# Performance work log

Measured on AMD Instinct MI355X. Metric: run time of the kernel, lower is better.

The kernel has to match this reference:

```python
import jax, jax.numpy as jnp
import numpy as np


def setup_inputs() -> dict:
    key = jax.random.key(0)
    ks = jax.random.split(key, 4)
    B, T, I, H = 64, 1024, 256, 512
    s = 1.0 / np.sqrt(I + H)  # torch Linear default init scale
    xs = jax.random.normal(ks[0], (B, T, I), dtype=jnp.float32)
    Wz = jax.random.uniform(ks[1], (I + H, H), jnp.float32, -s, s)
    Wr = jax.random.uniform(ks[2], (I + H, H), jnp.float32, -s, s)
    Wh = jax.random.uniform(ks[3], (I + H, H), jnp.float32, -s, s)
    bz = jnp.zeros((H,), jnp.float32)
    br = jnp.zeros((H,), jnp.float32)
    bh = jnp.zeros((H,), jnp.float32)
    return {"xs": xs, "Wz": Wz, "bz": bz, "Wr": Wr, "br": br, "Wh": Wh, "bh": bh}


def reference(xs, Wz, bz, Wr, br, Wh, bh):
    B, T, I = xs.shape
    H = Wz.shape[1]
    # split weights into input / hidden blocks so per-step work avoids concat
    Wz_x, Wz_h = Wz[:I], Wz[I:]
    Wr_x, Wr_h = Wr[:I], Wr[I:]
    Wh_x, Wh_h = Wh[:I], Wh[I:]
    # precompute all input projections in one big GEMM per gate: [B,T,H]
    xz = jnp.einsum('bti,ih->bth', xs, Wz_x) + bz
    xr = jnp.einsum('bti,ih->bth', xs, Wr_x) + br
    xh = jnp.einsum('bti,ih->bth', xs, Wh_x) + bh

    def step(h, inp):
        xz_t, xr_t, xh_t = inp
        zt = jax.nn.sigmoid(xz_t + h @ Wz_h)
        rt = jax.nn.sigmoid(xr_t + h @ Wr_h)
        ht = jnp.tanh(xh_t + (rt * h) @ Wh_h)
        h_next = (1 - zt) * h + zt * ht
        return h_next, h_next

    h0 = jnp.zeros((B, H), xs.dtype)
    # scan over time: inputs as [T, B, H]
    xs_t = (jnp.swapaxes(xz, 0, 1), jnp.swapaxes(xr, 0, 1), jnp.swapaxes(xh, 0, 1))
    h_last, hs = jax.lax.scan(step, h0, xs_t)
    return jnp.swapaxes(hs, 0, 1), h_last
```

## Files before the change

kernel.cpp:

```cpp
#include <hip/hip_runtime.h>
#include <cmath>

typedef __bf16 bf16x8 __attribute__((ext_vector_type(8)));
typedef float  f32x4  __attribute__((ext_vector_type(4)));
typedef unsigned long long u64;
typedef u64 u64x2 __attribute__((ext_vector_type(2)));

#define T_STEPS 1024
#define I_DIM   256
#define H_DIM   512
#define B_TOT   64
#define NBT     4
#define NCT     32
#define BT      16
#define CT      16
#define FDOM    64

__device__ __forceinline__ f32x4 mfma16(bf16x8 a, bf16x8 b, f32x4 c) {
    return __builtin_amdgcn_mfma_f32_16x16x32_bf16(a, b, c, 0, 0, 0);
}

__device__ __forceinline__ bf16x8 cvt8r(float4 a, float4 b) {
    bf16x8 f;
    f[0] = (__bf16)a.x; f[1] = (__bf16)a.y; f[2] = (__bf16)a.z; f[3] = (__bf16)a.w;
    f[4] = (__bf16)b.x; f[5] = (__bf16)b.y; f[6] = (__bf16)b.z; f[7] = (__bf16)b.w;
    return f;
}

__device__ __forceinline__ int ld_flag(const int* p) {
    return __hip_atomic_load(p, __ATOMIC_RELAXED, __HIP_MEMORY_SCOPE_AGENT);
}
__device__ __forceinline__ void st_flag(int* p, int v) {
    __hip_atomic_store(p, v, __ATOMIC_RELAXED, __HIP_MEMORY_SCOPE_AGENT);
}
__device__ __forceinline__ void st_u32(unsigned* p, unsigned v) {
    __hip_atomic_store(p, v, __ATOMIC_RELAXED, __HIP_MEMORY_SCOPE_AGENT);
}
__device__ __forceinline__ bf16x8 ld_frag16(const __bf16* p) {
    u64x2 v;
    v.x = __hip_atomic_load((const u64*)p,     __ATOMIC_RELAXED, __HIP_MEMORY_SCOPE_AGENT);
    v.y = __hip_atomic_load((const u64*)p + 1, __ATOMIC_RELAXED, __HIP_MEMORY_SCOPE_AGENT);
    return __builtin_bit_cast(bf16x8, v);
}

__device__ __forceinline__ void wait32(const int* fdom, int target) {
    const int* p = fdom + (threadIdx.x & 31);
    for (int g = 0; g < (1 << 22); ++g) {
        int v = ld_flag(p);
        if (__ballot(v >= target) == ~0ull) break;
    }
    asm volatile("" ::: "memory");
}

__device__ __forceinline__ void drain_vm() {
    __builtin_amdgcn_s_waitcnt(0x0f70);
}

__global__ __launch_bounds__(256, 1) void gru_persist(
    const float* __restrict__ xs,
    const float* __restrict__ Wz, const float* __restrict__ bz,
    const float* __restrict__ Wr, const float* __restrict__ br,
    const float* __restrict__ Wh, const float* __restrict__ bh,
    float* __restrict__ out,
    __bf16* hbuf, __bf16* rhbuf, int* flag_h, int* flag_r)
{
    const int bid  = blockIdx.x;
    const int i    = bid & (NBT - 1);
    const int j    = bid >> 2;
    const int tid  = threadIdx.x;
    const int w    = tid >> 6;
    const int lane = tid & 63;
    const int q    = lane >> 4;
    const int ln   = lane & 15;
    const int cb   = j * CT;

    __shared__ float red1[2][4][16][17];
    __shared__ float red2[4][16][17];
    __shared__ float z_lds[16][17];

    bf16x8 BZ[6], BR[6], BH[6];
    #pragma unroll
    for (int s = 0; s < 6; ++s) {
        int kk = w + 4 * s;
        int krow = kk * 32 + q * 8;
        bf16x8 fz, fr, fh;
        #pragma unroll
        for (int jj = 0; jj < 8; ++jj) {
            int off = (krow + jj) * H_DIM + cb + ln;
            fz[jj] = (__bf16)Wz[off];
            fr[jj] = (__bf16)Wr[off];
            fh[jj] = (__bf16)Wh[off];
        }
        BZ[s] = fz; BR[s] = fr; BH[s] = fh;
    }

    const int m = tid >> 4;
    const int c = tid & 15;
    const float bzc = bz[cb + c], brc = br[cb + c], bhc = bh[cb + c];
    float hprev = 0.0f;

    const float* xrow = xs + (size_t)(i * BT + ln) * T_STEPS * I_DIM;
    const int HB_P = NBT * BT * H_DIM;
    int* fh_dom = flag_h + i * FDOM;
    int* fr_dom = flag_r + i * FDOM;
    int* my_fh  = fh_dom + j;
    int* my_fr  = fr_dom + j;

    float4 xr[4];
    {
        const float* x0 = xrow;
        xr[0] = *(const float4*)(x0 + (w    ) * 32 + q * 8);
        xr[1] = *(const float4*)(x0 + (w    ) * 32 + q * 8 + 4);
        xr[2] = *(const float4*)(x0 + (w + 4) * 32 + q * 8);
        xr[3] = *(const float4*)(x0 + (w + 4) * 32 + q * 8 + 4);
    }

    for (int t = 0; t < T_STEPS; ++t) {
        const int p = t & 1, pp = p ^ 1;

        float4 xn[4];
        {
            int tn = (t + 1 < T_STEPS) ? t + 1 : t;
            const float* xp = xrow + (size_t)tn * I_DIM;
            xn[0] = *(const float4*)(xp + (w    ) * 32 + q * 8);
            xn[1] = *(const float4*)(xp + (w    ) * 32 + q * 8 + 4);
            xn[2] = *(const float4*)(xp + (w + 4) * 32 + q * 8);
            xn[3] = *(const float4*)(xp + (w + 4) * 32 + q * 8 + 4);
        }

        f32x4 accz = {0,0,0,0}, accr = {0,0,0,0}, acch = {0,0,0,0};

        {
            bf16x8 ax0 = cvt8r(xr[0], xr[1]);
            bf16x8 ax1 = cvt8r(xr[2], xr[3]);
            accz = mfma16(ax0, BZ[0], accz);
            accr = mfma16(ax0, BR[0], accr);
            acch = mfma16(ax0, BH[0], acch);
            accz = mfma16(ax1, BZ[1], accz);
            accr = mfma16(ax1, BR[1], accr);
            acch = mfma16(ax1, BH[1], acch);
        }

        if (t > 0) wait32(fh_dom, t);

        const __bf16* hb = hbuf + pp * HB_P + i * (BT * H_DIM) + ln * H_DIM;
        #pragma unroll
        for (int s = 2; s < 6; ++s) {
            int kk = w + 4 * s;
            bf16x8 ah = ld_frag16(hb + (kk - 8) * 32 + q * 8);
            accz = mfma16(ah, BZ[s], accz);
            accr = mfma16(ah, BR[s], accr);
        }

        #pragma unroll
        for (int r4 = 0; r4 < 4; ++r4) {
            red1[0][w][q*4 + r4][ln] = accz[r4];
            red1[1][w][q*4 + r4][ln] = accr[r4];
        }
        __syncthreads();

        {
            float pz = red1[0][0][m][c] + red1[0][1][m][c] + red1[0][2][m][c] + red1[0][3][m][c] + bzc;
            float pr = red1[1][0][m][c] + red1[1][1][m][c] + red1[1][2][m][c] + red1[1][3][m][c] + brc;
            float zv = 1.0f / (1.0f + __expf(-pz));
            float rv = 1.0f / (1.0f + __expf(-pr));
            z_lds[m][c] = zv;
            unsigned short v16 = __builtin_bit_cast(unsigned short, (__bf16)(rv * hprev));
            unsigned short nb  = (unsigned short)__shfl((int)v16, lane + 1);
            if (!(c & 1)) {
                unsigned pkd = (unsigned)v16 | ((unsigned)nb << 16);
                st_u32((unsigned*)(rhbuf + p * HB_P + i * (BT * H_DIM) + m * H_DIM + cb + c), pkd);
            }
            drain_vm();
            __syncthreads();
            if (tid == 0) st_flag(my_fr, t + 1);
        }

        wait32(fr_dom, t + 1);

        const __bf16* rb = rhbuf + p * HB_P + i * (BT * H_DIM) + ln * H_DIM;
        #pragma unroll
        for (int s = 2; s < 6; ++s) {
            int kk = w + 4 * s;
            bf16x8 ar = ld_frag16(rb + (kk - 8) * 32 + q * 8);
            acch = mfma16(ar, BH[s], acch);
        }

        #pragma unroll
        for (int r4 = 0; r4 < 4; ++r4)
            red2[w][q*4 + r4][ln] = acch[r4];
        __syncthreads();

        {
            float ph  = red2[0][m][c] + red2[1][m][c] + red2[2][m][c] + red2[3][m][c] + bhc;
            float e2  = __expf(2.0f * ph);
            float htl = (e2 - 1.0f) / (e2 + 1.0f);
            float zv2 = z_lds[m][c];
            float hn  = (1.0f - zv2) * hprev + zv2 * htl;
            hprev = hn;

            unsigned short v16 = __builtin_bit_cast(unsigned short, (__bf16)hn);
            unsigned short nb  = (unsigned short)__shfl((int)v16, lane + 1);
            if (!(c & 1)) {
                unsigned pkd = (unsigned)v16 | ((unsigned)nb << 16);
                st_u32((unsigned*)(hbuf + p * HB_P + i * (BT * H_DIM) + m * H_DIM + cb + c), pkd);
            }
            drain_vm();
            __syncthreads();
            if (tid == 0) st_flag(my_fh, t + 1);

            int bglob = i * BT + m;
            out[((size_t)bglob * T_STEPS + t) * H_DIM + cb + c] = hn;
            if (t == T_STEPS - 1)
                out[(size_t)B_TOT * T_STEPS * H_DIM + (size_t)bglob * H_DIM + cb + c] = hn;
        }

        xr[0] = xn[0]; xr[1] = xn[1]; xr[2] = xn[2]; xr[3] = xn[3];
    }
}

extern "C" void kernel_launch(void* const* d_in, const int* in_sizes, int n_in,
                              void* d_out, int out_size, void* d_ws, size_t ws_size,
                              hipStream_t stream)
{
    const float* xs = (const float*)d_in[0];
    const float* Wz = (const float*)d_in[1];
    const float* bz = (const float*)d_in[2];
    const float* Wr = (const float*)d_in[3];
    const float* br = (const float*)d_in[4];
    const float* Wh = (const float*)d_in[5];
    const float* bh = (const float*)d_in[6];
    float* out = (float*)d_out;

    __bf16* hbuf  = (__bf16*)d_ws;
    __bf16* rhbuf = hbuf + 2 * NBT * BT * H_DIM;
    int* flag_h = (int*)((char*)d_ws + 262144);
    int* flag_r = flag_h + NBT * FDOM;

    hipMemsetAsync(d_ws, 0, 262144 + 2 * NBT * FDOM * 4, stream);
    gru_persist<<<dim3(NBT * NCT), dim3(256), 0, stream>>>(
        xs, Wz, bz, Wr, br, Wh, bh, out, hbuf, rhbuf, flag_h, flag_r);
}
```

Baseline: 6.022 ms.

## Replace flag-based inter-block sync with tagged low-latency 64-bit data words

```diff
diff --git a/kernel.cpp b/kernel.cpp
--- a/kernel.cpp
+++ b/kernel.cpp
@@ -3,8 +3,9 @@
 
 typedef __bf16 bf16x8 __attribute__((ext_vector_type(8)));
 typedef float  f32x4  __attribute__((ext_vector_type(4)));
+typedef unsigned int u32;
 typedef unsigned long long u64;
-typedef u64 u64x2 __attribute__((ext_vector_type(2)));
+typedef u32 u32x4v __attribute__((ext_vector_type(4)));
 
 #define T_STEPS 1024
 #define I_DIM   256
@@ -14,7 +15,8 @@
 #define NCT     32
 #define BT      16
 #define CT      16
-#define FDOM    64
+#define WPB     (H_DIM / 2)
+#define LLSZ    (2 * NBT * BT * WPB)
 
 __device__ __forceinline__ f32x4 mfma16(bf16x8 a, bf16x8 b, f32x4 c) {
     return __builtin_amdgcn_mfma_f32_16x16x32_bf16(a, b, c, 0, 0, 0);
@@ -27,33 +29,35 @@
     return f;
 }
 
-__device__ __forceinline__ int ld_flag(const int* p) {
+__device__ __forceinline__ u64 ld_u64(const u64* p) {
     return __hip_atomic_load(p, __ATOMIC_RELAXED, __HIP_MEMORY_SCOPE_AGENT);
 }
-__device__ __forceinline__ void st_flag(int* p, int v) {
+__device__ __forceinline__ void st_u64(u64* p, u64 v) {
     __hip_atomic_store(p, v, __ATOMIC_RELAXED, __HIP_MEMORY_SCOPE_AGENT);
 }
-__device__ __forceinline__ void st_u32(unsigned* p, unsigned v) {
-    __hip_atomic_store(p, v, __ATOMIC_RELAXED, __HIP_MEMORY_SCOPE_AGENT);
-}
-__device__ __forceinline__ bf16x8 ld_frag16(const __bf16* p) {
-    u64x2 v;
-    v.x = __hip_atomic_load((const u64*)p,     __ATOMIC_RELAXED, __HIP_MEMORY_SCOPE_AGENT);
-    v.y = __hip_atomic_load((const u64*)p + 1, __ATOMIC_RELAXED, __HIP_MEMORY_SCOPE_AGENT);
-    return __builtin_bit_cast(bf16x8, v);
-}
-
-__device__ __forceinline__ void wait32(const int* fdom, int target) {
-    const int* p = fdom + (threadIdx.x & 31);
-    for (int g = 0; g < (1 << 22); ++g) {
-        int v = ld_flag(p);
-        if (__ballot(v >= target) == ~0ull) break;
-    }
-    asm volatile("" ::: "memory");
-}
-
-__device__ __forceinline__ void drain_vm() {
-    __builtin_amdgcn_s_waitcnt(0x0f70);
+
+__device__ __forceinline__ void ll_poll16(const u64* b0, const u64* b1,
+                                          const u64* b2, const u64* b3,
+                                          u32 tag, u64* wrd) {
+    for (int g = 0; g < (1 << 20); ++g) {
+        #pragma unroll
+        for (int k = 0; k < 4; ++k) {
+            wrd[0  + k] = ld_u64(b0 + k);
+            wrd[4  + k] = ld_u64(b1 + k);
+            wrd[8  + k] = ld_u64(b2 + k);
+            wrd[12 + k] = ld_u64(b3 + k);
+        }
+        bool ok = true;
+        #pragma unroll
+        for (int x = 0; x < 16; ++x) ok &= ((u32)(wrd[x] >> 32) == tag);
+        if (__ballot(ok) == ~0ull) break;
+    }
+}
+
+__device__ __forceinline__ bf16x8 frag_of(const u64* wrd) {
+    u32x4v d;
+    d.x = (u32)wrd[0]; d.y = (u32)wrd[1]; d.z = (u32)wrd[2]; d.w = (u32)wrd[3];
+    return __builtin_bit_cast(bf16x8, d);
 }
 
 __global__ __launch_bounds__(256, 1) void gru_persist(
@@ -62,7 +66,7 @@
     const float* __restrict__ Wr, const float* __restrict__ br,
     const float* __restrict__ Wh, const float* __restrict__ bh,
     float* __restrict__ out,
-    __bf16* hbuf, __bf16* rhbuf, int* flag_h, int* flag_r)
+    u64* hll, u64* rhll)
 {
     const int bid  = blockIdx.x;
     const int i    = bid & (NBT - 1);
@@ -76,7 +80,6 @@
 
     __shared__ float red1[2][4][16][17];
     __shared__ float red2[4][16][17];
-    __shared__ float z_lds[16][17];
 
     bf16x8 BZ[6], BR[6], BH[6];
     #pragma unroll
@@ -100,11 +103,8 @@
     float hprev = 0.0f;
 
     const float* xrow = xs + (size_t)(i * BT + ln) * T_STEPS * I_DIM;
-    const int HB_P = NBT * BT * H_DIM;
-    int* fh_dom = flag_h + i * FDOM;
-    int* fr_dom = flag_r + i * FDOM;
-    int* my_fh  = fh_dom + j;
-    int* my_fr  = fr_dom + j;
+
+    const int widx = q * 4;
 
     float4 xr[4];
     {
@@ -141,15 +141,20 @@
             acch = mfma16(ax1, BH[1], acch);
         }
 
-        if (t > 0) wait32(fh_dom, t);
-
-        const __bf16* hb = hbuf + pp * HB_P + i * (BT * H_DIM) + ln * H_DIM;
-        #pragma unroll
-        for (int s = 2; s < 6; ++s) {
-            int kk = w + 4 * s;
-            bf16x8 ah = ld_frag16(hb + (kk - 8) * 32 + q * 8);
-            accz = mfma16(ah, BZ[s], accz);
-            accr = mfma16(ah, BR[s], accr);
+        {
+            const u64* hb = hll + ((size_t)((pp * NBT + i) * BT) + ln) * WPB;
+            u64 wh[16];
+            ll_poll16(hb + (w     ) * 16 + widx,
+                      hb + (w +  4) * 16 + widx,
+                      hb + (w +  8) * 16 + widx,
+                      hb + (w + 12) * 16 + widx,
+                      (u32)t, wh);
+            #pragma unroll
+            for (int s = 0; s < 4; ++s) {
+                bf16x8 ah = frag_of(&wh[4 * s]);
+                accz = mfma16(ah, BZ[s + 2], accz);
+                accr = mfma16(ah, BR[s + 2], accr);
+            }
         }
 
         #pragma unroll
@@ -159,31 +164,31 @@
         }
         __syncthreads();
 
+        float zv;
         {
             float pz = red1[0][0][m][c] + red1[0][1][m][c] + red1[0][2][m][c] + red1[0][3][m][c] + bzc;
             float pr = red1[1][0][m][c] + red1[1][1][m][c] + red1[1][2][m][c] + red1[1][3][m][c] + brc;
-            float zv = 1.0f / (1.0f + __expf(-pz));
+            zv = 1.0f / (1.0f + __expf(-pz));
             float rv = 1.0f / (1.0f + __expf(-pr));
-            z_lds[m][c] = zv;
             unsigned short v16 = __builtin_bit_cast(unsigned short, (__bf16)(rv * hprev));
             unsigned short nb  = (unsigned short)__shfl((int)v16, lane + 1);
             if (!(c & 1)) {
-                unsigned pkd = (unsigned)v16 | ((unsigned)nb << 16);
-                st_u32((unsigned*)(rhbuf + p * HB_P + i * (BT * H_DIM) + m * H_DIM + cb + c), pkd);
+                u64 wrd = (u64)((u32)v16 | ((u32)nb << 16)) | ((u64)(u32)(t + 1) << 32);
+                st_u64(rhll + ((size_t)((p * NBT + i) * BT) + m) * WPB + ((cb + c) >> 1), wrd);
             }
-            drain_vm();
-            __syncthreads();
-            if (tid == 0) st_flag(my_fr, t + 1);
-        }
-
-        wait32(fr_dom, t + 1);
-
-        const __bf16* rb = rhbuf + p * HB_P + i * (BT * H_DIM) + ln * H_DIM;
-        #pragma unroll
-        for (int s = 2; s < 6; ++s) {
-            int kk = w + 4 * s;
-            bf16x8 ar = ld_frag16(rb + (kk - 8) * 32 + q * 8);
-            acch = mfma16(ar, BH[s], acch);
+        }
+
+        {
+            const u64* rb = rhll + ((size_t)((p * NBT + i) * BT) + ln) * WPB;
+            u64 wr_[16];
+            ll_poll16(rb + (w     ) * 16 + widx,
+                      rb + (w +  4) * 16 + widx,
+                      rb + (w +  8) * 16 + widx,
+                      rb + (w + 12) * 16 + widx,
+                      (u32)(t + 1), wr_);
+            #pragma unroll
+            for (int s = 0; s < 4; ++s)
+                acch = mfma16(frag_of(&wr_[4 * s]), BH[s + 2], acch);
         }
 
         #pragma unroll
@@ -195,19 +200,15 @@
             float ph  = red2[0][m][c] + red2[1][m][c] + red2[2][m][c] + red2[3][m][c] + bhc;
             float e2  = __expf(2.0f * ph);
             float htl = (e2 - 1.0f) / (e2 + 1.0f);
-            float zv2 = z_lds[m][c];
-            float hn  = (1.0f - zv2) * hprev + zv2 * htl;
+            float hn  = (1.0f - zv) * hprev + zv * htl;
             hprev = hn;
 
             unsigned short v16 = __builtin_bit_cast(unsigned short, (__bf16)hn);
             unsigned short nb  = (unsigned short)__shfl((int)v16, lane + 1);
             if (!(c & 1)) {
-                unsigned pkd = (unsigned)v16 | ((unsigned)nb << 16);
-                st_u32((unsigned*)(hbuf + p * HB_P + i * (BT * H_DIM) + m * H_DIM + cb + c), pkd);
+                u64 wrd = (u64)((u32)v16 | ((u32)nb << 16)) | ((u64)(u32)(t + 1) << 32);
+                st_u64(hll + ((size_t)((p * NBT + i) * BT) + m) * WPB + ((cb + c) >> 1), wrd);
             }
-            drain_vm();
-            __syncthreads();
-            if (tid == 0) st_flag(my_fh, t + 1);
 
             int bglob = i * BT + m;
             out[((size_t)bglob * T_STEPS + t) * H_DIM + cb + c] = hn;
@@ -232,12 +233,10 @@
     const float* bh = (const float*)d_in[6];
     float* out = (float*)d_out;
 
-    __bf16* hbuf  = (__bf16*)d_ws;
-    __bf16* rhbuf = hbuf + 2 * NBT * BT * H_DIM;
-    int* flag_h = (int*)((char*)d_ws + 262144);
-    int* flag_r = flag_h + NBT * FDOM;
-
-    hipMemsetAsync(d_ws, 0, 262144 + 2 * NBT * FDOM * 4, stream);
+    u64* hll  = (u64*)d_ws;
+    u64* rhll = hll + LLSZ;
+
+    hipMemsetAsync(d_ws, 0, 2 * LLSZ * sizeof(u64), stream);
     gru_persist<<<dim3(NBT * NCT), dim3(256), 0, stream>>>(
-        xs, Wz, bz, Wr, br, Wh, bh, out, hbuf, rhbuf, flag_h, flag_r);
-}
+        xs, Wz, bz, Wr, br, Wh, bh, out, hll, rhll);
+}
```

Result: slower. 8.729 ms (+44.9%).

## Specialize warps per gate to drop cross-warp K reductions

Applied to the files above, without the earlier changes.

```diff
diff --git a/kernel.cpp b/kernel.cpp
--- a/kernel.cpp
+++ b/kernel.cpp
@@ -3,6 +3,7 @@
 
 typedef __bf16 bf16x8 __attribute__((ext_vector_type(8)));
 typedef float  f32x4  __attribute__((ext_vector_type(4)));
+typedef unsigned int u32;
 typedef unsigned long long u64;
 typedef u64 u64x2 __attribute__((ext_vector_type(2)));
 
@@ -15,6 +16,7 @@
 #define BT      16
 #define CT      16
 #define FDOM    64
+#define HB_P    (NBT * BT * H_DIM)
 
 __device__ __forceinline__ f32x4 mfma16(bf16x8 a, bf16x8 b, f32x4 c) {
     return __builtin_amdgcn_mfma_f32_16x16x32_bf16(a, b, c, 0, 0, 0);
@@ -33,7 +35,7 @@
 __device__ __forceinline__ void st_flag(int* p, int v) {
     __hip_atomic_store(p, v, __ATOMIC_RELAXED, __HIP_MEMORY_SCOPE_AGENT);
 }
-__device__ __forceinline__ void st_u32(unsigned* p, unsigned v) {
+__device__ __forceinline__ void st_u32(u32* p, u32 v) {
     __hip_atomic_store(p, v, __ATOMIC_RELAXED, __HIP_MEMORY_SCOPE_AGENT);
 }
 __device__ __forceinline__ bf16x8 ld_frag16(const __bf16* p) {
@@ -52,8 +54,8 @@
     asm volatile("" ::: "memory");
 }
 
-__device__ __forceinline__ void drain_vm() {
-    __builtin_amdgcn_s_waitcnt(0x0f70);
+__device__ __forceinline__ void drain_all() {
+    asm volatile("s_waitcnt vmcnt(0) lgkmcnt(0)" ::: "memory");
 }
 
 __global__ __launch_bounds__(256, 1) void gru_persist(
@@ -74,148 +76,271 @@
     const int ln   = lane & 15;
     const int cb   = j * CT;
 
-    __shared__ float red1[2][4][16][17];
-    __shared__ float red2[4][16][17];
-    __shared__ float z_lds[16][17];
-
-    bf16x8 BZ[6], BR[6], BH[6];
-    #pragma unroll
-    for (int s = 0; s < 6; ++s) {
-        int kk = w + 4 * s;
-        int krow = kk * 32 + q * 8;
-        bf16x8 fz, fr, fh;
-        #pragma unroll
-        for (int jj = 0; jj < 8; ++jj) {
-            int off = (krow + jj) * H_DIM + cb + ln;
-            fz[jj] = (__bf16)Wz[off];
-            fr[jj] = (__bf16)Wr[off];
-            fh[jj] = (__bf16)Wh[off];
-        }
-        BZ[s] = fz; BR[s] = fr; BH[s] = fh;
-    }
-
-    const int m = tid >> 4;
-    const int c = tid & 15;
-    const float bzc = bz[cb + c], brc = br[cb + c], bhc = bh[cb + c];
-    float hprev = 0.0f;
+    __shared__ float zL[16][17];
+    __shared__ float pL[16][17];
+    __shared__ float hpL[16][17];
 
     const float* xrow = xs + (size_t)(i * BT + ln) * T_STEPS * I_DIM;
-    const int HB_P = NBT * BT * H_DIM;
     int* fh_dom = flag_h + i * FDOM;
     int* fr_dom = flag_r + i * FDOM;
     int* my_fh  = fh_dom + j;
     int* my_fr  = fr_dom + j;
 
-    float4 xr[4];
-    {
-        const float* x0 = xrow;
-        xr[0] = *(const float4*)(x0 + (w    ) * 32 + q * 8);
-        xr[1] = *(const float4*)(x0 + (w    ) * 32 + q * 8 + 4);
-        xr[2] = *(const float4*)(x0 + (w + 4) * 32 + q * 8);
-        xr[3] = *(const float4*)(x0 + (w + 4) * 32 + q * 8 + 4);
-    }
-
-    for (int t = 0; t < T_STEPS; ++t) {
-        const int p = t & 1, pp = p ^ 1;
-
-        float4 xn[4];
-        {
-            int tn = (t + 1 < T_STEPS) ? t + 1 : t;
-            const float* xp = xrow + (size_t)tn * I_DIM;
-            xn[0] = *(const float4*)(xp + (w    ) * 32 + q * 8);
-            xn[1] = *(const float4*)(xp + (w    ) * 32 + q * 8 + 4);
-            xn[2] = *(const float4*)(xp + (w + 4) * 32 + q * 8);
-            xn[3] = *(const float4*)(xp + (w + 4) * 32 + q * 8 + 4);
-        }
-
-        f32x4 accz = {0,0,0,0}, accr = {0,0,0,0}, acch = {0,0,0,0};
-
-        {
-            bf16x8 ax0 = cvt8r(xr[0], xr[1]);
-            bf16x8 ax1 = cvt8r(xr[2], xr[3]);
-            accz = mfma16(ax0, BZ[0], accz);
-            accr = mfma16(ax0, BR[0], accr);
-            acch = mfma16(ax0, BH[0], acch);
-            accz = mfma16(ax1, BZ[1], accz);
-            accr = mfma16(ax1, BR[1], accr);
-            acch = mfma16(ax1, BH[1], acch);
-        }
-
-        if (t > 0) wait32(fh_dom, t);
-
-        const __bf16* hb = hbuf + pp * HB_P + i * (BT * H_DIM) + ln * H_DIM;
-        #pragma unroll
-        for (int s = 2; s < 6; ++s) {
-            int kk = w + 4 * s;
-            bf16x8 ah = ld_frag16(hb + (kk - 8) * 32 + q * 8);
-            accz = mfma16(ah, BZ[s], accz);
-            accr = mfma16(ah, BR[s], accr);
-        }
-
-        #pragma unroll
-        for (int r4 = 0; r4 < 4; ++r4) {
-            red1[0][w][q*4 + r4][ln] = accz[r4];
-            red1[1][w][q*4 + r4][ln] = accr[r4];
-        }
-        __syncthreads();
-
-        {
-            float pz = red1[0][0][m][c] + red1[0][1][m][c] + red1[0][2][m][c] + red1[0][3][m][c] + bzc;
-            float pr = red1[1][0][m][c] + red1[1][1][m][c] + red1[1][2][m][c] + red1[1][3][m][c] + brc;
-            float zv = 1.0f / (1.0f + __expf(-pz));
-            float rv = 1.0f / (1.0f + __expf(-pr));
-            z_lds[m][c] = zv;
-            unsigned short v16 = __builtin_bit_cast(unsigned short, (__bf16)(rv * hprev));
-            unsigned short nb  = (unsigned short)__shfl((int)v16, lane + 1);
-            if (!(c & 1)) {
-                unsigned pkd = (unsigned)v16 | ((unsigned)nb << 16);
-                st_u32((unsigned*)(rhbuf + p * HB_P + i * (BT * H_DIM) + m * H_DIM + cb + c), pkd);
-            }
-            drain_vm();
-            __syncthreads();
-            if (tid == 0) st_flag(my_fr, t + 1);
-        }
-
-        wait32(fr_dom, t + 1);
-
-        const __bf16* rb = rhbuf + p * HB_P + i * (BT * H_DIM) + ln * H_DIM;
-        #pragma unroll
-        for (int s = 2; s < 6; ++s) {
-            int kk = w + 4 * s;
-            bf16x8 ar = ld_frag16(rb + (kk - 8) * 32 + q * 8);
-            acch = mfma16(ar, BH[s], acch);
-        }
-
-        #pragma unroll
-        for (int r4 = 0; r4 < 4; ++r4)
-            red2[w][q*4 + r4][ln] = acch[r4];
-        __syncthreads();
-
-        {
-            float ph  = red2[0][m][c] + red2[1][m][c] + red2[2][m][c] + red2[3][m][c] + bhc;
-            float e2  = __expf(2.0f * ph);
-            float htl = (e2 - 1.0f) / (e2 + 1.0f);
-            float zv2 = z_lds[m][c];
-            float hn  = (1.0f - zv2) * hprev + zv2 * htl;
-            hprev = hn;
-
-            unsigned short v16 = __builtin_bit_cast(unsigned short, (__bf16)hn);
-            unsigned short nb  = (unsigned short)__shfl((int)v16, lane + 1);
-            if (!(c & 1)) {
-                unsigned pkd = (unsigned)v16 | ((unsigned)nb << 16);
-                st_u32((unsigned*)(hbuf + p * HB_P + i * (BT * H_DIM) + m * H_DIM + cb + c), pkd);
-            }
-            drain_vm();
-            __syncthreads();
-            if (tid == 0) st_flag(my_fh, t + 1);
-
-            int bglob = i * BT + m;
-            out[((size_t)bglob * T_STEPS + t) * H_DIM + cb + c] = hn;
-            if (t == T_STEPS - 1)
-                out[(size_t)B_TOT * T_STEPS * H_DIM + (size_t)bglob * H_DIM + cb + c] = hn;
-        }
-
-        xr[0] = xn[0]; xr[1] = xn[1]; xr[2] = xn[2]; xr[3] = xn[3];
+    if (w == 0) {
+        bf16x8 WB[24];
+        #pragma unroll
+        for (int s = 0; s < 24; ++s) {
+            int krow = s * 32 + q * 8;
+            bf16x8 f;
+            #pragma unroll
+            for (int jj = 0; jj < 8; ++jj) f[jj] = (__bf16)Wr[(krow + jj) * H_DIM + cb + ln];
+            WB[s] = f;
+        }
+        const float bc = br[cb + ln];
+        float4 xst[16];
+        #pragma unroll
+        for (int c = 0; c < 8; ++c) {
+            xst[2*c]   = *(const float4*)(xrow + c * 32 + q * 8);
+            xst[2*c+1] = *(const float4*)(xrow + c * 32 + q * 8 + 4);
+        }
+        for (int t = 0; t < T_STEPS; ++t) {
+            const int p = t & 1, pp = p ^ 1;
+            bf16x8 xfr[8];
+            #pragma unroll
+            for (int c = 0; c < 8; ++c) xfr[c] = cvt8r(xst[2*c], xst[2*c+1]);
+
+            wait32(fh_dom, t);
+            const __bf16* hb = hbuf + pp * HB_P + i * (BT * H_DIM) + ln * H_DIM;
+            bf16x8 hf[16];
+            #pragma unroll
+            for (int s = 0; s < 16; ++s) hf[s] = ld_frag16(hb + s * 32 + q * 8);
+
+            f32x4 a0 = {0,0,0,0}, a1 = {0,0,0,0};
+            #pragma unroll
+            for (int c = 0; c < 8; ++c) {
+                if (c & 1) a1 = mfma16(xfr[c], WB[c], a1);
+                else       a0 = mfma16(xfr[c], WB[c], a0);
+            }
+            #pragma unroll
+            for (int s = 0; s < 16; ++s) {
+                if (s & 1) a1 = mfma16(hf[s], WB[8 + s], a1);
+                else       a0 = mfma16(hf[s], WB[8 + s], a0);
+            }
+            __bf16* rbase = rhbuf + p * HB_P + i * (BT * H_DIM);
+            #pragma unroll
+            for (int r4 = 0; r4 < 4; ++r4) {
+                int row = q * 4 + r4;
+                float pr = a0[r4] + a1[r4] + bc;
+                float rv = 1.0f / (1.0f + __expf(-pr));
+                float rh = rv * hpL[row][ln];
+                unsigned short v16 = __builtin_bit_cast(unsigned short, (__bf16)rh);
+                unsigned short nb  = (unsigned short)__shfl((int)v16, lane + 1);
+                if (!(ln & 1))
+                    st_u32((u32*)(rbase + row * H_DIM + cb + ln), (u32)v16 | ((u32)nb << 16));
+            }
+            __syncthreads();
+            if (lane == 0) st_flag(my_fr, t + 1);
+            {
+                const float* xp = xrow + (size_t)((t + 1 < T_STEPS) ? t + 1 : t) * I_DIM;
+                #pragma unroll
+                for (int c = 0; c < 8; ++c) {
+                    xst[2*c]   = *(const float4*)(xp + c * 32 + q * 8);
+                    xst[2*c+1] = *(const float4*)(xp + c * 32 + q * 8 + 4);
+                }
+            }
+            __syncthreads();
+        }
+    } else if (w == 1) {
+        bf16x8 WB[24];
+        #pragma unroll
+        for (int s = 0; s < 24; ++s) {
+            int krow = s * 32 + q * 8;
+            bf16x8 f;
+            #pragma unroll
+            for (int jj = 0; jj < 8; ++jj) f[jj] = (__bf16)Wz[(krow + jj) * H_DIM + cb + ln];
+            WB[s] = f;
+        }
+        const float bc = bz[cb + ln];
+        float4 xst[16];
+        #pragma unroll
+        for (int c = 0; c < 8; ++c) {
+            xst[2*c]   = *(const float4*)(xrow + c * 32 + q * 8);
+            xst[2*c+1] = *(const float4*)(xrow + c * 32 + q * 8 + 4);
+        }
+        for (int t = 0; t < T_STEPS; ++t) {
+            const int pp = (t & 1) ^ 1;
+            bf16x8 xfr[8];
+            #pragma unroll
+            for (int c = 0; c < 8; ++c) xfr[c] = cvt8r(xst[2*c], xst[2*c+1]);
+
+            wait32(fh_dom, t);
+            const __bf16* hb = hbuf + pp * HB_P + i * (BT * H_DIM) + ln * H_DIM;
+            bf16x8 hf[16];
+            #pragma unroll
+            for (int s = 0; s < 16; ++s) hf[s] = ld_frag16(hb + s * 32 + q * 8);
+
+            __syncthreads();
+
+            f32x4 a0 = {0,0,0,0}, a1 = {0,0,0,0};
+            #pragma unroll
+            for (int c = 0; c < 8; ++c) {
+                if (c & 1) a1 = mfma16(xfr[c], WB[c], a1);
+                else       a0 = mfma16(xfr[c], WB[c], a0);
+            }
+            #pragma unroll
+            for (int s = 0; s < 16; ++s) {
+                if (s & 1) a1 = mfma16(hf[s], WB[8 + s], a1);
+                else       a0 = mfma16(hf[s], WB[8 + s], a0);
+            }
+            #pragma unroll
+            for (int r4 = 0; r4 < 4; ++r4) {
+                float pz = a0[r4] + a1[r4] + bc;
+                zL[q * 4 + r4][ln] = 1.0f / (1.0f + __expf(-pz));
+            }
+            __syncthreads();
+            {
+                const float* xp = xrow + (size_t)((t + 1 < T_STEPS) ? t + 1 : t) * I_DIM;
+                #pragma unroll
+                for (int c = 0; c < 8; ++c) {
+                    xst[2*c]   = *(const float4*)(xp + c * 32 + q * 8);
+                    xst[2*c+1] = *(const float4*)(xp + c * 32 + q * 8 + 4);
+                }
+            }
+        }
+    } else if (w == 2) {
+        bf16x8 WB[12];
+        #pragma unroll
+        for (int c = 0; c < 4; ++c) {
+            int krow = c * 32 + q * 8;
+            bf16x8 f;
+            #pragma unroll
+            for (int jj = 0; jj < 8; ++jj) f[jj] = (__bf16)Wh[(krow + jj) * H_DIM + cb + ln];
+            WB[c] = f;
+        }
+        #pragma unroll
+        for (int s = 0; s < 8; ++s) {
+            int krow = (8 + s) * 32 + q * 8;
+            bf16x8 f;
+            #pragma unroll
+            for (int jj = 0; jj < 8; ++jj) f[jj] = (__bf16)Wh[(krow + jj) * H_DIM + cb + ln];
+            WB[4 + s] = f;
+        }
+        float4 xst[8];
+        #pragma unroll
+        for (int c = 0; c < 4; ++c) {
+            xst[2*c]   = *(const float4*)(xrow + c * 32 + q * 8);
+            xst[2*c+1] = *(const float4*)(xrow + c * 32 + q * 8 + 4);
+        }
+        for (int t = 0; t < T_STEPS; ++t) {
+            const int p = t & 1;
+            f32x4 acc = {0,0,0,0};
+            #pragma unroll
+            for (int c = 0; c < 4; ++c) acc = mfma16(cvt8r(xst[2*c], xst[2*c+1]), WB[c], acc);
+
+            __syncthreads();
+            wait32(fr_dom, t + 1);
+            const __bf16* rb = rhbuf + p * HB_P + i * (BT * H_DIM) + ln * H_DIM;
+            bf16x8 rf[8];
+            #pragma unroll
+            for (int s = 0; s < 8; ++s) rf[s] = ld_frag16(rb + s * 32 + q * 8);
+            #pragma unroll
+            for (int s = 0; s < 8; ++s) acc = mfma16(rf[s], WB[4 + s], acc);
+            #pragma unroll
+            for (int r4 = 0; r4 < 4; ++r4) pL[q * 4 + r4][ln] = acc[r4];
+            __syncthreads();
+            {
+                const float* xp = xrow + (size_t)((t + 1 < T_STEPS) ? t + 1 : t) * I_DIM;
+                #pragma unroll
+                for (int c = 0; c < 4; ++c) {
+                    xst[2*c]   = *(const float4*)(xp + c * 32 + q * 8);
+                    xst[2*c+1] = *(const float4*)(xp + c * 32 + q * 8 + 4);
+                }
+            }
+        }
+    } else {
+        bf16x8 WB[12];
+        #pragma unroll
+        for (int c = 0; c < 4; ++c) {
+            int krow = (4 + c) * 32 + q * 8;
+            bf16x8 f;
+            #pragma unroll
+            for (int jj = 0; jj < 8; ++jj) f[jj] = (__bf16)Wh[(krow + jj) * H_DIM + cb + ln];
+            WB[c] = f;
+        }
+        #pragma unroll
+        for (int s = 0; s < 8; ++s) {
+            int krow = (16 + s) * 32 + q * 8;
+            bf16x8 f;
+            #pragma unroll
+            for (int jj = 0; jj < 8; ++jj) f[jj] = (__bf16)Wh[(krow + jj) * H_DIM + cb + ln];
+            WB[4 + s] = f;
+        }
+        const float bc = bh[cb + ln];
+        float hpv[4] = {0.0f, 0.0f, 0.0f, 0.0f};
+        #pragma unroll
+        for (int r4 = 0; r4 < 4; ++r4) hpL[q * 4 + r4][ln] = 0.0f;
+        float4 xst[8];
+        #pragma unroll
+        for (int c = 0; c < 4; ++c) {
+            xst[2*c]   = *(const float4*)(xrow + (4 + c) * 32 + q * 8);
+            xst[2*c+1] = *(const float4*)(xrow + (4 + c) * 32 + q * 8 + 4);
+        }
+        for (int t = 0; t < T_STEPS; ++t) {
+            const int p = t & 1;
+            f32x4 acc = {0,0,0,0};
+            #pragma unroll
+            for (int c = 0; c < 4; ++c) acc = mfma16(cvt8r(xst[2*c], xst[2*c+1]), WB[c], acc);
+
+            __syncthreads();
+            wait32(fr_dom, t + 1);
+            const __bf16* rb = rhbuf + p * HB_P + i * (BT * H_DIM) + ln * H_DIM;
+            bf16x8 rf[8];
+            #pragma unroll
+            for (int s = 0; s < 8; ++s) rf[s] = ld_frag16(rb + (8 + s) * 32 + q * 8);
+            #pragma unroll
+            for (int s = 0; s < 8; ++s) acc = mfma16(rf[s], WB[4 + s], acc);
+            __syncthreads();
+
+            __bf16* hbw = hbuf + p * HB_P + i * (BT * H_DIM);
+            float hn4[4];
+            #pragma unroll
+            for (int r4 = 0; r4 < 4; ++r4) {
+                int row = q * 4 + r4;
+                float ph = acc[r4] + pL[row][ln] + bc;
+                float e2 = __expf(2.0f * ph);
+                float ht = (e2 - 1.0f) / (e2 + 1.0f);
+                float zv = zL[row][ln];
+                float hn = (1.0f - zv) * hpv[r4] + zv * ht;
+                hpv[r4] = hn; hn4[r4] = hn;
+                hpL[row][ln] = hn;
+            }
+            #pragma unroll
+            for (int r4 = 0; r4 < 4; ++r4) {
+                int row = q * 4 + r4;
+                unsigned short v16 = __builtin_bit_cast(unsigned short, (__bf16)hn4[r4]);
+                unsigned short nb  = (unsigned short)__shfl((int)v16, lane + 1);
+                if (!(ln & 1))
+                    st_u32((u32*)(hbw + row * H_DIM + cb + ln), (u32)v16 | ((u32)nb << 16));
+            }
+            drain_all();
+            if (lane == 0) st_flag(my_fh, t + 1);
+            #pragma unroll
+            for (int r4 = 0; r4 < 4; ++r4) {
+                int row = q * 4 + r4;
+                int bglob = i * BT + row;
+                out[((size_t)bglob * T_STEPS + t) * H_DIM + cb + ln] = hn4[r4];
+                if (t == T_STEPS - 1)
+                    out[(size_t)B_TOT * T_STEPS * H_DIM + (size_t)bglob * H_DIM + cb + ln] = hn4[r4];
+            }
+            {
+                const float* xp = xrow + (size_t)((t + 1 < T_STEPS) ? t + 1 : t) * I_DIM;
+                #pragma unroll
+                for (int c = 0; c < 4; ++c) {
+                    xst[2*c]   = *(const float4*)(xp + (4 + c) * 32 + q * 8);
+                    xst[2*c+1] = *(const float4*)(xp + (4 + c) * 32 + q * 8 + 4);
+                }
+            }
+        }
     }
 }
 
@@ -233,7 +358,7 @@
     float* out = (float*)d_out;
 
     __bf16* hbuf  = (__bf16*)d_ws;
-    __bf16* rhbuf = hbuf + 2 * NBT * BT * H_DIM;
+    __bf16* rhbuf = hbuf + 2 * HB_P;
     int* flag_h = (int*)((char*)d_ws + 262144);
     int* flag_r = flag_h + NBT * FDOM;
 
```

New measurement: 9.235 ms. +53.3%, slower.
